# Optimization experiments

Measured on AMD Instinct MI355X. Metric: run time of the kernel, lower is better.

Reference implementation:

```python
import jax, jax.numpy as jnp
import numpy as np

STEPS = 100
RATE = 200
THR = 1.0
BETA = 0.0
SG_ALPHA = 2.0  # snntorch default ATan surrogate alpha


@jax.custom_vjp
def spike_fn(x):
    # heaviside spike with atan surrogate gradient (snntorch default)
    return (x > 0).astype(x.dtype)

def _spike_fwd(x):
    return spike_fn(x), x

def _spike_bwd(x, g):
    grad = (SG_ALPHA / 2.0) / (1.0 + (jnp.pi / 2.0 * SG_ALPHA * x) ** 2)
    return (g * grad,)

spike_fn.defvjp(_spike_fwd, _spike_bwd)


def conv2d(x, w):
    # x: [B,C,H,W], w: [O,I,K,K], VALID, stride 1, no bias
    return jax.lax.conv_general_dilated(
        x, w, window_strides=(1, 1), padding='VALID',
        dimension_numbers=('NCHW', 'OIHW', 'NCHW'))


def avg_pool2(x):
    s = jax.lax.reduce_window(x, 0.0, jax.lax.add, (1, 1, 2, 2), (1, 1, 2, 2), 'VALID')
    return s * 0.25


def lif(cur, mem):
    # snntorch Leaky, reset_mechanism='subtract'; reset signal is detached
    reset = jax.lax.stop_gradient((mem > THR).astype(cur.dtype))
    mem = BETA * mem + cur - reset * THR
    spk = spike_fn(mem - THR)
    return spk, mem


def setup_inputs() -> dict:
    key = jax.random.key(0)
    k1, k2, k3, k4 = jax.random.split(key, 4)
    B, C, H, W = 64, 3, 32, 32
    x = jax.random.uniform(k1, (B, C, H, W), dtype=jnp.float32)
    # kaiming-uniform-ish init scales (exact values irrelevant for correctness baseline)
    W_in = jax.random.normal(k2, (32, 3, 5, 5), dtype=jnp.float32) * 0.1
    W_h1 = jax.random.normal(k3, (64, 32, 5, 5), dtype=jnp.float32) * 0.05
    W_h2 = jax.random.normal(k4, (10, 1600), dtype=jnp.float32) * 0.02
    return {"x": x, "W_in": W_in, "W_h1": W_h1, "W_h2": W_h2}


def reference(x, W_in, W_h1, W_h2):
    B, C, H, W = x.shape
    K = W_in.shape[2]
    # poisson spike train: [steps, B, C, H, W]
    rescale = RATE / STEPS
    rand = jax.random.uniform(jax.random.key(1), (STEPS, B, C, H, W), dtype=x.dtype)
    spikes = (rand < x * rescale).astype(x.dtype)

    H1 = (H - K + 1) // 2; W1 = (W - K + 1) // 2           # after conv1+pool
    H2 = (H1 - K + 1) // 2; W2 = (W1 - K + 1) // 2          # after conv2+pool
    mem0 = (jnp.zeros((B, W_in.shape[0], H1, W1), x.dtype),
            jnp.zeros((B, W_h1.shape[0], H2, W2), x.dtype),
            jnp.zeros((B, W_h2.shape[0]), x.dtype))

    def step(carry, s):
        memin, memh1, memh2 = carry
        spkin, memin = lif(avg_pool2(conv2d(s, W_in)), memin)
        spkh1, memh1 = lif(avg_pool2(conv2d(spkin, W_h1)), memh1)
        flat = spkh1.reshape(spkh1.shape[0], -1)
        spkh2, memh2 = lif(flat @ W_h2.T, memh2)
        return (memin, memh1, memh2), (spkh2, memh2)

    _, (out_spikes, memh2_mem) = jax.lax.scan(step, mem0, spikes)
    return out_spikes, memh2_mem
```

## Files before the change

kernel.cpp:

```cpp
#include <hip/hip_runtime.h>
#include <stdint.h>


#define NSTEPS 100
#define NB 64
#define CAPF1 524288u
#define CAPF2 262144u

typedef short bf16x8 __attribute__((ext_vector_type(8)));
typedef float f32x4 __attribute__((ext_vector_type(4)));

__device__ __forceinline__ uint32_t rotl32(uint32_t v, uint32_t r) {
  return (v << r) | (v >> (32u - r));
}

__device__ __forceinline__ void threefry2x32(uint32_t k0, uint32_t k1,
                                             uint32_t& x0, uint32_t& x1) {
  uint32_t k2 = k0 ^ k1 ^ 0x1BD11BDAu;
  x0 += k0; x1 += k1;
#define TF_R(r) { x0 += x1; x1 = rotl32(x1, r); x1 ^= x0; }
  TF_R(13u) TF_R(15u) TF_R(26u) TF_R(6u)
  x0 += k1; x1 += k2 + 1u;
  TF_R(17u) TF_R(29u) TF_R(16u) TF_R(24u)
  x0 += k2; x1 += k0 + 2u;
  TF_R(13u) TF_R(15u) TF_R(26u) TF_R(6u)
  x0 += k0; x1 += k1 + 3u;
  TF_R(17u) TF_R(29u) TF_R(16u) TF_R(24u)
  x0 += k1; x1 += k2 + 4u;
  TF_R(13u) TF_R(15u) TF_R(26u) TF_R(6u)
  x0 += k2; x1 += k0 + 5u;
#undef TF_R
}

__device__ __forceinline__ double fold_pool_w(const float* W, int base, int pos) {
  int iy = pos / 6, ix = pos % 6;
  double w = 0.0;
  for (int dy = 0; dy < 2; ++dy) {
    int ky = iy - dy; if (ky < 0 || ky > 4) continue;
    for (int dx = 0; dx < 2; ++dx) {
      int kx = ix - dx; if (kx < 0 || kx > 4) continue;
      w += (double)W[base + ky * 5 + kx];
    }
  }
  return w;
}

__device__ __forceinline__ uint16_t f2bf(float x) {
  uint32_t u = __float_as_uint(x);
  uint32_t r = (u + 0x7fffu + ((u >> 16) & 1u)) >> 16;
  return (uint16_t)r;
}

__global__ __launch_bounds__(256) void prep_all(const float* __restrict__ W_in,
                                                const float* __restrict__ W_h1,
                                                double* __restrict__ W1R,
                                                double* __restrict__ W2R,
                                                uint16_t* __restrict__ WB1,
                                                uint16_t* __restrict__ WB2,
                                                float* __restrict__ EPS,
                                                uint32_t* __restrict__ cnt) {
  if (blockIdx.x < 654) {
    int e = blockIdx.x * 256 + threadIdx.x;
    if (e < 3456) {
      int oj = e & 7, c = (e >> 3) % 3, pos = ((e >> 3) / 3) % 36, og = (e >> 3) / 108;
      int oc = og * 8 + oj;
      W1R[e] = fold_pool_w(W_in, (oc * 3 + c) * 25, pos);
    } else if (e < 77184) {
      int e2 = e - 3456;
      int oj = e2 & 15, pos = (e2 >> 4) % 36, c = ((e2 >> 4) / 36) % 32, og = e2 / 18432;
      int oc = og * 16 + oj;
      W2R[e2] = fold_pool_w(W_h1, (oc * 32 + c) * 25, pos);
    } else if (e < 93568) {
      int e3 = e - 77184;
      int j = e3 & 7, lane = (e3 >> 3) & 63, nt = (e3 >> 9) & 1, ks = (e3 >> 10) & 3, hl = e3 >> 12;
      int k = ks * 32 + (lane >> 4) * 8 + j;
      int oc = nt * 16 + (lane & 15);
      uint16_t val = 0;
      if (k < 108) {
        int c = k / 36, pos = k % 36;
        double w = fold_pool_w(W_in, (oc * 3 + c) * 25, pos);
        uint16_t hi = f2bf((float)w);
        if (hl == 0) val = hi;
        else {
          float hif = __uint_as_float(((uint32_t)hi) << 16);
          val = f2bf((float)(w - (double)hif));
        }
      }
      WB1[e3] = val;
    } else if (e < 167296) {
      int e4 = e - 93568;
      int j = e4 & 7, lane = (e4 >> 3) & 63, nt = (e4 >> 9) & 3, pos = e4 >> 11;
      int oc = nt * 16 + (lane & 15);
      int c  = (lane >> 4) * 8 + j;
      double w = fold_pool_w(W_h1, (oc * 32 + c) * 25, pos);
      uint16_t hi = f2bf((float)w);
      float hif = __uint_as_float(((uint32_t)hi) << 16);
      uint16_t lo = f2bf((float)(w - (double)hif));
      WB2[e4] = hi;
      WB2[73728 + e4] = lo;
    } else if (e < 167298) {
      cnt[e - 167296] = 0;
    }
  } else {
    int wid = threadIdx.x >> 6, lane = threadIdx.x & 63;
    int o = (blockIdx.x - 654) * 4 + wid;
    const double u24 = 5.9604644775390625e-08;
    double s = 0.0;
    if (o < 32) {
      for (int t = lane; t < 108; t += 64) {
        int pos = t / 3, c = t % 3;
        s += fabs(fold_pool_w(W_in, (o * 3 + c) * 25, pos));
      }
    } else {
      int oc = o - 32;
      for (int t = lane; t < 1152; t += 64) {
        int c = t / 36, pos = t % 36;
        s += fabs(fold_pool_w(W_h1, (oc * 32 + c) * 25, pos));
      }
    }
    #pragma unroll
    for (int off = 32; off > 0; off >>= 1) s += __shfl_xor(s, off);
    if (lane == 0)
      EPS[o] = (o < 32) ? (float)(s * (108.0 * u24 * 6.0) * 0.25)
                        : (float)(s * (1152.0 * u24 * 6.0) * 0.25);
  }
}

__global__ __launch_bounds__(256) void gen_spikes(const float* __restrict__ x,
                                                  uint32_t* __restrict__ rowm) {
  int id = blockIdx.x * 4 + (threadIdx.x >> 6);
  int lane = threadIdx.x & 63;
  int rp = id & 15, c = (id >> 4) % 3, tb = id / 48;
  int pix = rp * 64 + lane;
  int b = tb & 63;
  uint32_t i = (uint32_t)((tb * 3 + c) * 1024 + pix);
  uint32_t x0 = 0u, x1 = i;
  threefry2x32(0u, 1u, x0, x1);
  uint32_t bits = x0 ^ x1;
  float u = __uint_as_float((bits >> 9) | 0x3f800000u) - 1.0f;
  float xv = x[(b * 3 + c) * 1024 + pix];
  unsigned long long mask = __ballot(u < 2.0f * xv);
  if (lane == 0) ((unsigned long long*)rowm)[id] = mask;
}

__global__ __launch_bounds__(256) void conv1_mfma(const uint32_t* __restrict__ rowm,
                                                  const uint16_t* __restrict__ WB1,
                                                  const float* __restrict__ EPS,
                                                  uint32_t* __restrict__ A1w,
                                                  uint32_t* __restrict__ B1w,
                                                  uint32_t* __restrict__ cnt,
                                                  uint32_t* __restrict__ list1) {
  __shared__ uint32_t sR[4][96];
  const int tid = threadIdx.x;
  const int wid = tid >> 6, lane = tid & 63;
  const int tb = blockIdx.x * 4 + wid;
  const int q = lane >> 4, ln = lane & 15;

  for (int i = lane; i < 96; i += 64) sR[wid][i] = rowm[tb * 96 + i];

  const float eps0 = EPS[ln];
  const float eps1 = EPS[16 + ln];

  bf16x8 bf[2][4][2];
  #pragma unroll
  for (int hl = 0; hl < 2; ++hl)
    #pragma unroll
    for (int ks = 0; ks < 4; ++ks)
      #pragma unroll
      for (int nt = 0; nt < 2; ++nt)
        bf[hl][ks][nt] =
            *(const bf16x8*)(WB1 + ((((hl * 4 + ks) * 2 + nt) * 64 + lane) * 8));

  const int wl = lane;
  const int qq = wl >> 2, rr = wl & 3;

  for (int mt = 0; mt < 13; ++mt) {
    int p = mt * 16 + ln;
    int pc = p < 196 ? p : 195;
    int oh = pc / 14, ow = pc % 14;
    uint64_t seg0 = 0, seg1 = 0, seg2 = 0;
    #pragma unroll
    for (int iy = 0; iy < 6; ++iy) {
      seg0 |= (uint64_t)((sR[wid][0 * 32 + 2 * oh + iy] >> (2 * ow)) & 0x3fu) << (6 * iy);
      seg1 |= (uint64_t)((sR[wid][1 * 32 + 2 * oh + iy] >> (2 * ow)) & 0x3fu) << (6 * iy);
      seg2 |= (uint64_t)((sR[wid][2 * 32 + 2 * oh + iy] >> (2 * ow)) & 0x3fu) << (6 * iy);
    }
    uint64_t lo = seg0 | (seg1 << 36);
    uint64_t hi = (seg1 >> 28) | (seg2 << 8);
    uint32_t wz[4] = {(uint32_t)lo, (uint32_t)(lo >> 32),
                      (uint32_t)hi, (uint32_t)(hi >> 32)};

    f32x4 acc0 = (f32x4)(0.0f), acc1 = (f32x4)(0.0f);
    #pragma unroll
    for (int ks = 0; ks < 4; ++ks) {
      uint32_t byte = (wz[ks] >> (q * 8)) & 0xffu;
      union { uint32_t u[4]; bf16x8 v; } a;
      #pragma unroll
      for (int i = 0; i < 4; ++i)
        a.u[i] = (((byte >> (2 * i)) & 1u) ? 0x3F80u : 0u) |
                 (((byte >> (2 * i + 1)) & 1u) ? 0x3F800000u : 0u);
      acc0 = __builtin_amdgcn_mfma_f32_16x16x32_bf16(a.v, bf[0][ks][0], acc0, 0, 0, 0);
      acc0 = __builtin_amdgcn_mfma_f32_16x16x32_bf16(a.v, bf[1][ks][0], acc0, 0, 0, 0);
      acc1 = __builtin_amdgcn_mfma_f32_16x16x32_bf16(a.v, bf[0][ks][1], acc1, 0, 0, 0);
      acc1 = __builtin_amdgcn_mfma_f32_16x16x32_bf16(a.v, bf[1][ks][1], acc1, 0, 0, 0);
    }

    unsigned long long bA0[4], bA1[4], bB0[4], bB1[4], bF0[4], bF1[4];
    #pragma unroll
    for (int r = 0; r < 4; ++r) {
      float c0 = acc0[r] * 0.25f;
      float c1 = acc1[r] * 0.25f;
      bA0[r] = __ballot(c0 > 1.0f);
      bB0[r] = __ballot(c0 > 2.0f);
      bF0[r] = __ballot(fabsf(c0 - 1.0f) <= eps0 || fabsf(c0 - 2.0f) <= eps0);
      bA1[r] = __ballot(c1 > 1.0f);
      bB1[r] = __ballot(c1 > 2.0f);
      bF1[r] = __ballot(fabsf(c1 - 1.0f) <= eps1 || fabsf(c1 - 2.0f) <= eps1);
    }

    int pw = mt * 16 + wl;
    if (wl < 16 && pw < 196) {
#define SEL(B) (rr == 0 ? B[0] : rr == 1 ? B[1] : rr == 2 ? B[2] : B[3])
      uint32_t wA = (uint32_t)((SEL(bA0) >> (qq * 16)) & 0xffffull) |
                    ((uint32_t)((SEL(bA1) >> (qq * 16)) & 0xffffull) << 16);
      uint32_t wB = (uint32_t)((SEL(bB0) >> (qq * 16)) & 0xffffull) |
                    ((uint32_t)((SEL(bB1) >> (qq * 16)) & 0xffffull) << 16);
      uint32_t wF = (uint32_t)((SEL(bF0) >> (qq * 16)) & 0xffffull) |
                    ((uint32_t)((SEL(bF1) >> (qq * 16)) & 0xffffull) << 16);
#undef SEL
      uint32_t idx = (uint32_t)(tb * 196 + pw);
      A1w[idx] = wA;
      B1w[idx] = wB;
      if (wF) {
        uint32_t n = (uint32_t)__popc(wF);
        uint32_t slot = atomicAdd(&cnt[0], n);
        uint32_t base = idx * 32u;
        while (wF) {
          int bit = __ffs(wF) - 1; wF &= wF - 1;
          if (slot < CAPF1) list1[slot] = base + (uint32_t)bit;
          ++slot;
        }
      }
    }
  }
}

__global__ __launch_bounds__(64) void fix1b(const uint32_t* __restrict__ cnt,
                                            const uint32_t* __restrict__ list,
                                            const uint32_t* __restrict__ rowm,
                                            const double* __restrict__ W1R,
                                            uint32_t* __restrict__ A1w,
                                            uint32_t* __restrict__ B1w) {
  uint32_t total = cnt[0]; if (total > CAPF1) total = CAPF1;
  for (uint32_t i = blockIdx.x * 64 + threadIdx.x; i < total; i += gridDim.x * 64) {
    uint32_t e = list[i];
    uint32_t x = e >> 5;
    int oc = (int)(e & 31u);
    int tb = (int)(x / 196), p = (int)(x % 196);
    int oh = p / 14, ow = p % 14;
    int og = oc >> 3, oj = oc & 7;
    const uint32_t* R = rowm + (size_t)tb * 96;
    double acc = 0.0;
    for (int iy = 0; iy < 6; ++iy)
      for (int ix = 0; ix < 6; ++ix)
        for (int c = 0; c < 3; ++c) {
          double bd = (double)((R[c * 32 + 2 * oh + iy] >> (2 * ow + ix)) & 1u);
          acc = fma(bd, W1R[og * 864 + (iy * 6 + ix) * 24 + c * 8 + oj], acc);
        }
    float cur = (float)(acc * 0.25);
    uint32_t m = 1u << oc;
    if (cur > 1.0f) atomicOr(&A1w[x], m); else atomicAnd(&A1w[x], ~m);
    if (cur > 2.0f) atomicOr(&B1w[x], m); else atomicAnd(&B1w[x], ~m);
  }
}

__global__ __launch_bounds__(64) void scan1(const uint32_t* __restrict__ A1w,
                                            const uint32_t* __restrict__ B1w,
                                            uint32_t* __restrict__ mask1) {
  int chain = blockIdx.x * 64 + threadIdx.x;
  if (chain >= NB * 196) return;
  int b = chain / 196, p = chain % 196;
  const size_t stride = (size_t)NB * 196;
  size_t base = (size_t)b * 196 + p;
  uint32_t prev = 0;
  #pragma unroll
  for (int seg = 0; seg < 4; ++seg) {
    uint32_t Abuf[25], Bbuf[25];
    size_t sb = base + (size_t)(seg * 25) * stride;
    #pragma unroll
    for (int i = 0; i < 25; ++i) {
      Abuf[i] = A1w[sb + i * stride];
      Bbuf[i] = B1w[sb + i * stride];
    }
    #pragma unroll
    for (int i = 0; i < 25; ++i) {
      uint32_t s = (Abuf[i] & ~prev) | (Bbuf[i] & prev);
      mask1[sb + i * stride] = s;
      prev = s;
    }
  }
}

#define CONV2_EPILOG(ACC, TBV)                                                \
  {                                                                           \
    const int w = lane;                                                       \
    const int pw = w >> 1, hfw = w & 1;                                       \
    _Pragma("unroll")                                                         \
    for (int mt2 = 0; mt2 < 2; ++mt2) {                                       \
      const int pt = pw - mt2 * 16;                                           \
      const bool wvalid = (w < 50) && (pt >= 0) && (pt < 16) && (pw < 25);    \
      const int qw = (pt & 15) >> 2, rw = pt & 3;                             \
      uint32_t wA = 0, wB = 0, wF = 0;                                        \
      _Pragma("unroll")                                                       \
      for (int nt = 0; nt < 4; ++nt) {                                        \
        unsigned long long bA[4], bB[4], bF[4];                               \
        _Pragma("unroll")                                                     \
        for (int reg = 0; reg < 4; ++reg) {                                   \
          float c = ACC[mt2 * 4 + nt][reg] * 0.25f;                           \
          float e = epsv[nt];                                                 \
          bA[reg] = __ballot(c > 1.0f);                                       \
          bB[reg] = __ballot(c > 2.0f);                                       \
          bF[reg] = __ballot(fabsf(c - 1.0f) <= e || fabsf(c - 2.0f) <= e);   \
        }                                                                     \
        if (wvalid && (nt >> 1) == hfw) {                                     \
          const int sh = (nt & 1) * 16;                                       \
          unsigned long long sA = rw == 0 ? bA[0] : rw == 1 ? bA[1] : rw == 2 ? bA[2] : bA[3]; \
          unsigned long long sB = rw == 0 ? bB[0] : rw == 1 ? bB[1] : rw == 2 ? bB[2] : bB[3]; \
          unsigned long long sF = rw == 0 ? bF[0] : rw == 1 ? bF[1] : rw == 2 ? bF[2] : bF[3]; \
          wA |= (uint32_t)((sA >> (qw * 16)) & 0xffffull) << sh;              \
          wB |= (uint32_t)((sB >> (qw * 16)) & 0xffffull) << sh;              \
          wF |= (uint32_t)((sF >> (qw * 16)) & 0xffffull) << sh;              \
        }                                                                     \
      }                                                                       \
      if (wvalid) {                                                           \
        uint32_t idx = (uint32_t)((TBV) * 25 + pw) * 2 + hfw;                 \
        A2w[idx] = wA;                                                        \
        B2w[idx] = wB;                                                        \
        if (wF) {                                                             \
          uint32_t n = (uint32_t)__popc(wF);                                  \
          uint32_t slot = atomicAdd(&cnt[1], n);                              \
          uint32_t base2 = idx * 32u;                                         \
          while (wF) {                                                        \
            int bit = __ffs(wF) - 1; wF &= wF - 1;                            \
            if (slot < CAPF2) list2[slot] = base2 + (uint32_t)bit;            \
            ++slot;                                                           \
          }                                                                   \
        }                                                                     \
      }                                                                       \
    }                                                                         \
  }

__global__ __launch_bounds__(256, 3) void conv2_mfma(const uint32_t* __restrict__ mask1,
                                                     const uint16_t* __restrict__ WB,
                                                     const float* __restrict__ EPS,
                                                     uint32_t* __restrict__ A2w,
                                                     uint32_t* __restrict__ B2w,
                                                     uint32_t* __restrict__ cnt,
                                                     uint32_t* __restrict__ list2) {
  __shared__ uint32_t sM[8 * 196];
  const int tid = threadIdx.x;
  const int wid = tid >> 6, lane = tid & 63;
  const int tb0 = blockIdx.x * 8 + wid * 2;

  for (int i = lane; i < 392; i += 64)
    sM[wid * 392 + i] = mask1[(size_t)tb0 * 196 + i];

  const int q  = lane >> 4;
  const int ln = lane & 15;
  float epsv[4];
  #pragma unroll
  for (int nt = 0; nt < 4; ++nt) epsv[nt] = EPS[32 + nt * 16 + ln];

  const int p0 = ln;
  const int p1 = 16 + ln;
  const bool v1 = (p1 < 25);
  const int oh0 = p0 / 5, ow0 = p0 % 5;
  const int p1c = v1 ? p1 : 0;
  const int oh1 = p1c / 5, ow1 = p1c % 5;

  f32x4 accA[8], accB[8];
  #pragma unroll
  for (int i = 0; i < 8; ++i) { accA[i] = (f32x4)(0.0f); accB[i] = (f32x4)(0.0f); }

  const uint32_t* sW0 = &sM[wid * 392];
  const uint32_t* sW1 = sW0 + 196;

  for (int iy = 0; iy < 6; ++iy) {
    #pragma unroll
    for (int ix = 0; ix < 6; ++ix) {
      const int pos = iy * 6 + ix;
      const int o0 = (2 * oh0 + iy) * 14 + 2 * ow0 + ix;
      const int o1 = (2 * oh1 + iy) * 14 + 2 * ow1 + ix;
      uint32_t w00 = sW0[o0];
      uint32_t w01 = v1 ? sW0[o1] : 0u;
      uint32_t w10 = sW1[o0];
      uint32_t w11 = v1 ? sW1[o1] : 0u;
      uint32_t b00 = (w00 >> (q * 8)) & 0xffu;
      uint32_t b01 = (w01 >> (q * 8)) & 0xffu;
      uint32_t b10 = (w10 >> (q * 8)) & 0xffu;
      uint32_t b11 = (w11 >> (q * 8)) & 0xffu;
      union { uint32_t u[4]; bf16x8 v; } a00, a01, a10, a11;
      #pragma unroll
      for (int i = 0; i < 4; ++i) {
        a00.u[i] = (((b00 >> (2 * i)) & 1u) ? 0x3F80u : 0u) |
                   (((b00 >> (2 * i + 1)) & 1u) ? 0x3F800000u : 0u);
        a01.u[i] = (((b01 >> (2 * i)) & 1u) ? 0x3F80u : 0u) |
                   (((b01 >> (2 * i + 1)) & 1u) ? 0x3F800000u : 0u);
        a10.u[i] = (((b10 >> (2 * i)) & 1u) ? 0x3F80u : 0u) |
                   (((b10 >> (2 * i + 1)) & 1u) ? 0x3F800000u : 0u);
        a11.u[i] = (((b11 >> (2 * i)) & 1u) ? 0x3F80u : 0u) |
                   (((b11 >> (2 * i + 1)) & 1u) ? 0x3F800000u : 0u);
      }
      const uint16_t* bhi_base = WB + (size_t)pos * 2048 + lane * 8;
      const uint16_t* blo_base = bhi_base + 73728;
      #pragma unroll
      for (int nt = 0; nt < 4; ++nt) {
        bf16x8 bhi = *(const bf16x8*)(bhi_base + nt * 512);
        bf16x8 blo = *(const bf16x8*)(blo_base + nt * 512);
        accA[nt] = __builtin_amdgcn_mfma_f32_16x16x32_bf16(a00.v, bhi, accA[nt], 0, 0, 0);
        accA[nt] = __builtin_amdgcn_mfma_f32_16x16x32_bf16(a00.v, blo, accA[nt], 0, 0, 0);
        accA[4 + nt] = __builtin_amdgcn_mfma_f32_16x16x32_bf16(a01.v, bhi, accA[4 + nt], 0, 0, 0);
        accA[4 + nt] = __builtin_amdgcn_mfma_f32_16x16x32_bf16(a01.v, blo, accA[4 + nt], 0, 0, 0);
        accB[nt] = __builtin_amdgcn_mfma_f32_16x16x32_bf16(a10.v, bhi, accB[nt], 0, 0, 0);
        accB[nt] = __builtin_amdgcn_mfma_f32_16x16x32_bf16(a10.v, blo, accB[nt], 0, 0, 0);
        accB[4 + nt] = __builtin_amdgcn_mfma_f32_16x16x32_bf16(a11.v, bhi, accB[4 + nt], 0, 0, 0);
        accB[4 + nt] = __builtin_amdgcn_mfma_f32_16x16x32_bf16(a11.v, blo, accB[4 + nt], 0, 0, 0);
      }
    }
  }

  CONV2_EPILOG(accA, tb0)
  CONV2_EPILOG(accB, (tb0 + 1))
}

__global__ __launch_bounds__(64) void fix2b(const uint32_t* __restrict__ cnt,
                                            const uint32_t* __restrict__ list,
                                            const uint32_t* __restrict__ mask1,
                                            const double* __restrict__ W2R,
                                            uint32_t* __restrict__ A2w,
                                            uint32_t* __restrict__ B2w) {
  uint32_t total = cnt[1]; if (total > CAPF2) total = CAPF2;
  for (uint32_t i = blockIdx.x * 64 + threadIdx.x; i < total; i += gridDim.x * 64) {
    uint32_t e = list[i];
    uint32_t wi = e >> 5;
    int bit = (int)(e & 31u);
    uint32_t x = wi >> 1;
    int oc = (int)((wi & 1u) * 32u) + bit;
    int tb = (int)(x / 25), p = (int)(x % 25);
    int oh = p / 5, ow = p % 5;
    int og = oc >> 4, oj = oc & 15;
    const uint32_t* M = mask1 + (size_t)tb * 196;
    double acc = 0.0;
    for (int c = 0; c < 32; ++c)
      for (int iy = 0; iy < 6; ++iy)
        for (int ix = 0; ix < 6; ++ix) {
          uint32_t mm = M[(2 * oh + iy) * 14 + 2 * ow + ix];
          double bd = (double)((mm >> c) & 1u);
          acc = fma(bd, W2R[og * 18432 + c * 576 + (iy * 6 + ix) * 16 + oj], acc);
        }
    float cur = (float)(acc * 0.25);
    uint32_t m = 1u << bit;
    if (cur > 1.0f) atomicOr(&A2w[wi], m); else atomicAnd(&A2w[wi], ~m);
    if (cur > 2.0f) atomicOr(&B2w[wi], m); else atomicAnd(&B2w[wi], ~m);
  }
}

__global__ __launch_bounds__(64) void scan2(const uint64_t* __restrict__ A2q,
                                            const uint64_t* __restrict__ B2q,
                                            uint64_t* __restrict__ mask2) {
  int chain = blockIdx.x * 64 + threadIdx.x;
  if (chain >= NB * 25) return;
  int b = chain / 25, p = chain % 25;
  const size_t stride = (size_t)NB * 25;
  size_t base = (size_t)b * 25 + p;
  uint64_t prev = 0;
  #pragma unroll
  for (int seg = 0; seg < 4; ++seg) {
    uint64_t Abuf[25], Bbuf[25];
    size_t sb = base + (size_t)(seg * 25) * stride;
    #pragma unroll
    for (int i = 0; i < 25; ++i) {
      Abuf[i] = A2q[sb + i * stride];
      Bbuf[i] = B2q[sb + i * stride];
    }
    #pragma unroll
    for (int i = 0; i < 25; ++i) {
      uint64_t s = (Abuf[i] & ~prev) | (Bbuf[i] & prev);
      mask2[sb + i * stride] = s;
      prev = s;
    }
  }
}

__global__ __launch_bounds__(256) void fc_kernel(const uint64_t* __restrict__ mask2,
                                                 const float* __restrict__ W2,
                                                 float* __restrict__ cur3) {
  int gid = blockIdx.x * 256 + threadIdx.x;
  if (gid >= NSTEPS * NB * 80) return;
  int tb = gid / 80, r = gid % 80;
  int o = r >> 3, s = r & 7;
  const uint64_t* m = mask2 + (size_t)tb * 25;
  const float* w = W2 + o * 1600 + s * 200;

  uint64_t mw[25];
  #pragma unroll
  for (int p = 0; p < 25; ++p) mw[p] = m[p];

  const int oc0 = s * 8;
  double acc0 = 0.0, acc1 = 0.0;
  #pragma unroll
  for (int j = 0; j < 8; ++j) {
    const float* wj = w + j * 25;
    double a = 0.0;
    #pragma unroll
    for (int p = 0; p < 25; ++p) {
      double bd = (double)((mw[p] >> (oc0 + j)) & 1ull);
      a = fma(bd, (double)wj[p], a);
    }
    if (j & 1) acc1 += a; else acc0 += a;
  }
  double acc = acc0 + acc1;
  acc += __shfl_xor(acc, 4);
  acc += __shfl_xor(acc, 2);
  acc += __shfl_xor(acc, 1);
  if (s == 0) cur3[tb * 10 + o] = (float)acc;
}

__global__ __launch_bounds__(64) void lif3_kernel(const float* __restrict__ cur3,
                                                  float* __restrict__ out) {
  int bo = blockIdx.x * 64 + threadIdx.x;
  if (bo >= NB * 10) return;
  float prev = 0.0f;
  #pragma unroll
  for (int seg = 0; seg < 4; ++seg) {
    float cbuf[25];
    #pragma unroll
    for (int i = 0; i < 25; ++i) cbuf[i] = cur3[(seg * 25 + i) * 640 + bo];
    #pragma unroll
    for (int i = 0; i < 25; ++i) {
      int t = seg * 25 + i;
      float mem = cbuf[i] - prev;
      bool s = mem > 1.0f;
      out[t * 640 + bo] = s ? 1.0f : 0.0f;
      out[NSTEPS * 640 + t * 640 + bo] = mem;
      prev = s ? 1.0f : 0.0f;
    }
  }
}

extern "C" void kernel_launch(void* const* d_in, const int* in_sizes, int n_in,
                              void* d_out, int out_size, void* d_ws, size_t ws_size,
                              hipStream_t stream) {
  const float* x    = (const float*)d_in[0];
  const float* W_in = (const float*)d_in[1];
  const float* W_h1 = (const float*)d_in[2];
  const float* W_h2 = (const float*)d_in[3];
  float* out = (float*)d_out;

  unsigned char* ws = (unsigned char*)d_ws;
  double*   W1R   = (double*)(ws + 0);
  double*   W2R   = (double*)(ws + 27648);
  uint16_t* WB1   = (uint16_t*)(ws + 617472);
  uint16_t* WB2   = (uint16_t*)(ws + 650240);
  float*    EPS   = (float*)(ws + 945152);
  uint32_t* cnt   = (uint32_t*)(ws + 945536);
  uint32_t* rowm  = (uint32_t*)(ws + 945664);
  uint32_t* A1w   = (uint32_t*)(ws + 3403264);
  uint32_t* B1w   = (uint32_t*)(ws + 8420864);
  uint32_t* mask1 = (uint32_t*)(ws + 13438464);
  uint32_t* A2w   = (uint32_t*)(ws + 18456064);
  uint32_t* B2w   = (uint32_t*)(ws + 19736064);
  uint64_t* mask2 = (uint64_t*)(ws + 21016064);
  float*    cur3  = (float*)(ws + 22296064);
  uint32_t* list1 = (uint32_t*)(ws + 22552064);
  uint32_t* list2 = (uint32_t*)(ws + 24649216);

  prep_all<<<678, 256, 0, stream>>>(W_in, W_h1, W1R, W2R, WB1, WB2, EPS, cnt);
  gen_spikes<<<76800, 256, 0, stream>>>(x, rowm);
  conv1_mfma<<<1600, 256, 0, stream>>>(rowm, WB1, EPS, A1w, B1w, cnt, list1);
  fix1b<<<1024, 64, 0, stream>>>(cnt, list1, rowm, W1R, A1w, B1w);
  scan1<<<(NB * 196 + 63) / 64, 64, 0, stream>>>(A1w, B1w, mask1);
  conv2_mfma<<<800, 256, 0, stream>>>(mask1, WB2, EPS, A2w, B2w, cnt, list2);
  fix2b<<<1024, 64, 0, stream>>>(cnt, list2, mask1, W2R, A2w, B2w);
  scan2<<<(NB * 25 + 63) / 64, 64, 0, stream>>>((const uint64_t*)A2w,
                                                (const uint64_t*)B2w, mask2);
  fc_kernel<<<(NSTEPS * NB * 80 + 255) / 256, 256, 0, stream>>>(mask2, W_h2, cur3);
  lif3_kernel<<<10, 64, 0, stream>>>(cur3, out);
}
```

Before: 349.8 us.

## Split fp64 fix-up dot products across lane groups and merge prep with spike generation

The fp64 recheck kernels for near-threshold conv outputs now give each list entry to a group of 8 (conv1) or 16 (conv2) lanes. The lanes split the reduction and combine partial sums with xor shuffles, instead of one thread doing all 108 or 1152 terms serially. The weight prep kernel and the Poisson spike generation kernel are fused into one launch, which removes a kernel boundary. The fix-up kernels use larger blocks and fewer entries per pass, so the summation order changes slightly but stays in double precision.

```diff
diff --git a/kernel.cpp b/kernel.cpp
--- a/kernel.cpp
+++ b/kernel.cpp
@@ -51,14 +51,32 @@
   return (uint16_t)r;
 }
 
-__global__ __launch_bounds__(256) void prep_all(const float* __restrict__ W_in,
+__global__ __launch_bounds__(256) void prep_gen(const float* __restrict__ W_in,
                                                 const float* __restrict__ W_h1,
+                                                const float* __restrict__ x,
                                                 double* __restrict__ W1R,
                                                 double* __restrict__ W2R,
                                                 uint16_t* __restrict__ WB1,
                                                 uint16_t* __restrict__ WB2,
                                                 float* __restrict__ EPS,
-                                                uint32_t* __restrict__ cnt) {
+                                                uint32_t* __restrict__ cnt,
+                                                uint32_t* __restrict__ rowm) {
+  if (blockIdx.x >= 678) {
+    int id = (blockIdx.x - 678) * 4 + (threadIdx.x >> 6);
+    int lane = threadIdx.x & 63;
+    int rp = id & 15, c = (id >> 4) % 3, tb = id / 48;
+    int pix = rp * 64 + lane;
+    int b = tb & 63;
+    uint32_t i = (uint32_t)((tb * 3 + c) * 1024 + pix);
+    uint32_t x0 = 0u, x1 = i;
+    threefry2x32(0u, 1u, x0, x1);
+    uint32_t bits = x0 ^ x1;
+    float u = __uint_as_float((bits >> 9) | 0x3f800000u) - 1.0f;
+    float xv = x[(b * 3 + c) * 1024 + pix];
+    unsigned long long mask = __ballot(u < 2.0f * xv);
+    if (lane == 0) ((unsigned long long*)rowm)[id] = mask;
+    return;
+  }
   if (blockIdx.x < 654) {
     int e = blockIdx.x * 256 + threadIdx.x;
     if (e < 3456) {
@@ -126,23 +144,6 @@
   }
 }
 
-__global__ __launch_bounds__(256) void gen_spikes(const float* __restrict__ x,
-                                                  uint32_t* __restrict__ rowm) {
-  int id = blockIdx.x * 4 + (threadIdx.x >> 6);
-  int lane = threadIdx.x & 63;
-  int rp = id & 15, c = (id >> 4) % 3, tb = id / 48;
-  int pix = rp * 64 + lane;
-  int b = tb & 63;
-  uint32_t i = (uint32_t)((tb * 3 + c) * 1024 + pix);
-  uint32_t x0 = 0u, x1 = i;
-  threefry2x32(0u, 1u, x0, x1);
-  uint32_t bits = x0 ^ x1;
-  float u = __uint_as_float((bits >> 9) | 0x3f800000u) - 1.0f;
-  float xv = x[(b * 3 + c) * 1024 + pix];
-  unsigned long long mask = __ballot(u < 2.0f * xv);
-  if (lane == 0) ((unsigned long long*)rowm)[id] = mask;
-}
-
 __global__ __launch_bounds__(256) void conv1_mfma(const uint32_t* __restrict__ rowm,
                                                   const uint16_t* __restrict__ WB1,
                                                   const float* __restrict__ EPS,
@@ -245,14 +246,17 @@
   }
 }
 
-__global__ __launch_bounds__(64) void fix1b(const uint32_t* __restrict__ cnt,
-                                            const uint32_t* __restrict__ list,
-                                            const uint32_t* __restrict__ rowm,
-                                            const double* __restrict__ W1R,
-                                            uint32_t* __restrict__ A1w,
-                                            uint32_t* __restrict__ B1w) {
+__global__ __launch_bounds__(256) void fix1c(const uint32_t* __restrict__ cnt,
+                                             const uint32_t* __restrict__ list,
+                                             const uint32_t* __restrict__ rowm,
+                                             const double* __restrict__ W1R,
+                                             uint32_t* __restrict__ A1w,
+                                             uint32_t* __restrict__ B1w) {
   uint32_t total = cnt[0]; if (total > CAPF1) total = CAPF1;
-  for (uint32_t i = blockIdx.x * 64 + threadIdx.x; i < total; i += gridDim.x * 64) {
+  const uint32_t g = blockIdx.x * 32 + (threadIdx.x >> 3);
+  const int l = threadIdx.x & 7;
+  const uint32_t gstride = gridDim.x * 32;
+  for (uint32_t i = g; i < total; i += gstride) {
     uint32_t e = list[i];
     uint32_t x = e >> 5;
     int oc = (int)(e & 31u);
@@ -261,16 +265,21 @@
     int og = oc >> 3, oj = oc & 7;
     const uint32_t* R = rowm + (size_t)tb * 96;
     double acc = 0.0;
-    for (int iy = 0; iy < 6; ++iy)
-      for (int ix = 0; ix < 6; ++ix)
-        for (int c = 0; c < 3; ++c) {
-          double bd = (double)((R[c * 32 + 2 * oh + iy] >> (2 * ow + ix)) & 1u);
-          acc = fma(bd, W1R[og * 864 + (iy * 6 + ix) * 24 + c * 8 + oj], acc);
-        }
-    float cur = (float)(acc * 0.25);
-    uint32_t m = 1u << oc;
-    if (cur > 1.0f) atomicOr(&A1w[x], m); else atomicAnd(&A1w[x], ~m);
-    if (cur > 2.0f) atomicOr(&B1w[x], m); else atomicAnd(&B1w[x], ~m);
+    for (int t = l; t < 108; t += 8) {
+      int pos = t / 3, c = t - pos * 3;
+      int iy = pos / 6, ix = pos - iy * 6;
+      double bd = (double)((R[c * 32 + 2 * oh + iy] >> (2 * ow + ix)) & 1u);
+      acc = fma(bd, W1R[og * 864 + pos * 24 + c * 8 + oj], acc);
+    }
+    acc += __shfl_xor(acc, 1);
+    acc += __shfl_xor(acc, 2);
+    acc += __shfl_xor(acc, 4);
+    if (l == 0) {
+      float cur = (float)(acc * 0.25);
+      uint32_t m = 1u << oc;
+      if (cur > 1.0f) atomicOr(&A1w[x], m); else atomicAnd(&A1w[x], ~m);
+      if (cur > 2.0f) atomicOr(&B1w[x], m); else atomicAnd(&B1w[x], ~m);
+    }
   }
 }
 
@@ -433,14 +442,17 @@
   CONV2_EPILOG(accB, (tb0 + 1))
 }
 
-__global__ __launch_bounds__(64) void fix2b(const uint32_t* __restrict__ cnt,
-                                            const uint32_t* __restrict__ list,
-                                            const uint32_t* __restrict__ mask1,
-                                            const double* __restrict__ W2R,
-                                            uint32_t* __restrict__ A2w,
-                                            uint32_t* __restrict__ B2w) {
+__global__ __launch_bounds__(256) void fix2c(const uint32_t* __restrict__ cnt,
+                                             const uint32_t* __restrict__ list,
+                                             const uint32_t* __restrict__ mask1,
+                                             const double* __restrict__ W2R,
+                                             uint32_t* __restrict__ A2w,
+                                             uint32_t* __restrict__ B2w) {
   uint32_t total = cnt[1]; if (total > CAPF2) total = CAPF2;
-  for (uint32_t i = blockIdx.x * 64 + threadIdx.x; i < total; i += gridDim.x * 64) {
+  const uint32_t g = blockIdx.x * 16 + (threadIdx.x >> 4);
+  const int l = threadIdx.x & 15;
+  const uint32_t gstride = gridDim.x * 16;
+  for (uint32_t i = g; i < total; i += gstride) {
     uint32_t e = list[i];
     uint32_t wi = e >> 5;
     int bit = (int)(e & 31u);
@@ -451,17 +463,23 @@
     int og = oc >> 4, oj = oc & 15;
     const uint32_t* M = mask1 + (size_t)tb * 196;
     double acc = 0.0;
-    for (int c = 0; c < 32; ++c)
-      for (int iy = 0; iy < 6; ++iy)
-        for (int ix = 0; ix < 6; ++ix) {
-          uint32_t mm = M[(2 * oh + iy) * 14 + 2 * ow + ix];
-          double bd = (double)((mm >> c) & 1u);
-          acc = fma(bd, W2R[og * 18432 + c * 576 + (iy * 6 + ix) * 16 + oj], acc);
-        }
-    float cur = (float)(acc * 0.25);
-    uint32_t m = 1u << bit;
-    if (cur > 1.0f) atomicOr(&A2w[wi], m); else atomicAnd(&A2w[wi], ~m);
-    if (cur > 2.0f) atomicOr(&B2w[wi], m); else atomicAnd(&B2w[wi], ~m);
+    for (int t = l; t < 1152; t += 16) {
+      int c = t / 36, pos = t - c * 36;
+      int iy = pos / 6, ix = pos - iy * 6;
+      uint32_t mm = M[(2 * oh + iy) * 14 + 2 * ow + ix];
+      double bd = (double)((mm >> c) & 1u);
+      acc = fma(bd, W2R[og * 18432 + c * 576 + pos * 16 + oj], acc);
+    }
+    acc += __shfl_xor(acc, 1);
+    acc += __shfl_xor(acc, 2);
+    acc += __shfl_xor(acc, 4);
+    acc += __shfl_xor(acc, 8);
+    if (l == 0) {
+      float cur = (float)(acc * 0.25);
+      uint32_t m = 1u << bit;
+      if (cur > 1.0f) atomicOr(&A2w[wi], m); else atomicAnd(&A2w[wi], ~m);
+      if (cur > 2.0f) atomicOr(&B2w[wi], m); else atomicAnd(&B2w[wi], ~m);
+    }
   }
 }
 
@@ -575,13 +593,13 @@
   uint32_t* list1 = (uint32_t*)(ws + 22552064);
   uint32_t* list2 = (uint32_t*)(ws + 24649216);
 
-  prep_all<<<678, 256, 0, stream>>>(W_in, W_h1, W1R, W2R, WB1, WB2, EPS, cnt);
-  gen_spikes<<<76800, 256, 0, stream>>>(x, rowm);
+  prep_gen<<<678 + 76800, 256, 0, stream>>>(W_in, W_h1, x, W1R, W2R, WB1, WB2,
+                                            EPS, cnt, rowm);
   conv1_mfma<<<1600, 256, 0, stream>>>(rowm, WB1, EPS, A1w, B1w, cnt, list1);
-  fix1b<<<1024, 64, 0, stream>>>(cnt, list1, rowm, W1R, A1w, B1w);
+  fix1c<<<1024, 256, 0, stream>>>(cnt, list1, rowm, W1R, A1w, B1w);
   scan1<<<(NB * 196 + 63) / 64, 64, 0, stream>>>(A1w, B1w, mask1);
   conv2_mfma<<<800, 256, 0, stream>>>(mask1, WB2, EPS, A2w, B2w, cnt, list2);
-  fix2b<<<1024, 64, 0, stream>>>(cnt, list2, mask1, W2R, A2w, B2w);
+  fix2c<<<1024, 256, 0, stream>>>(cnt, list2, mask1, W2R, A2w, B2w);
   scan2<<<(NB * 25 + 63) / 64, 64, 0, stream>>>((const uint64_t*)A2w,
                                                 (const uint64_t*)B2w, mask2);
   fc_kernel<<<(NSTEPS * NB * 80 + 255) / 256, 256, 0, stream>>>(mask2, W_h2, cur3);
```

New measurement: 299.3 us. 14.4% less time.
